# Kernel tuning notes

Hardware: AMD Instinct MI355X
Metric: run time of the kernel (lower is better)

Reference implementation:

```python
import jax, jax.numpy as jnp
import numpy as np

REL_DIM = 1024
NUM_HEADS = 16
HEAD_DIM = REL_DIM // NUM_HEADS
REL_EMB_DIM = 256
B, K = 32, 512
SCALE = 1.0 / float(np.sqrt(HEAD_DIM))


def setup_inputs() -> dict:
    key = jax.random.key(0)
    ks = jax.random.split(key, 7)
    s = 1.0 / float(np.sqrt(REL_DIM))
    return {
        "h_R": jax.random.normal(ks[0], (B, K, REL_DIM), dtype=jnp.float32),
        "R": jax.random.normal(ks[1], (K, REL_EMB_DIM), dtype=jnp.float32),
        "W_q": jax.random.normal(ks[2], (REL_DIM, REL_DIM), dtype=jnp.float32) * s,
        "W_k": jax.random.normal(ks[3], (REL_DIM, REL_DIM), dtype=jnp.float32) * s,
        "W_v": jax.random.normal(ks[4], (REL_DIM, REL_DIM), dtype=jnp.float32) * s,
        "W_o": jax.random.normal(ks[5], (REL_DIM, REL_DIM), dtype=jnp.float32) * s,
        "w_sim": jax.random.normal(ks[6], (NUM_HEADS,), dtype=jnp.float32) * 0.1,
    }


def reference(h_R, R, W_q, W_k, W_v, W_o, w_sim):
    Bb, Kk, _ = h_R.shape
    H, D = NUM_HEADS, HEAD_DIM
    # torch Linear: x @ W.T ; then split heads -> (B, H, K, D)
    def proj(x, W):
        return jnp.einsum('bkd,ed->bke', x, W).reshape(Bb, Kk, H, D).transpose(0, 2, 1, 3)
    q = proj(h_R, W_q)
    k = proj(h_R, W_k)
    v = proj(h_R, W_v)
    attn = jnp.einsum('bhqd,bhkd->bhqk', q, k) * SCALE
    # cosine-similarity bias (batch-independent): (H, K, K)
    R_norm = R / jnp.maximum(jnp.linalg.norm(R, axis=-1, keepdims=True), 1e-12)
    sim = R_norm @ R_norm.T  # (K, K)
    bias = w_sim[:, None, None] * sim[None]  # (H, K, K)
    attn = attn + bias[None]
    alpha = jax.nn.softmax(attn, axis=-1)
    out = jnp.einsum('bhqk,bhkd->bhqd', alpha, v)
    out = out.transpose(0, 2, 1, 3).reshape(Bb, Kk, H * D)
    return jnp.einsum('bkd,ed->bke', out, W_o)
```

## Files before the change

kernel.cpp:

```cpp
#include <hip/hip_runtime.h>

#define SEQK 512
#define NH 16
#define HD 64
#define RD 1024
#define BBATCH 32
#define QK_SCALE 0.125f

typedef unsigned short u16;
using bf16x8 = __attribute__((ext_vector_type(8))) short;
using f32x4  = __attribute__((ext_vector_type(4))) float;

__device__ __forceinline__ u16 f2bf(float f) {
  unsigned u = __float_as_uint(f);
  u += 0x7FFFu + ((u >> 16) & 1u);
  return (u16)(u >> 16);
}
__device__ __forceinline__ u16 f2bf_fast(float f) {
  return (u16)((__float_as_uint(f) + 0x8000u) >> 16);
}
__device__ __forceinline__ float bf2f(u16 v) {
  return __uint_as_float(((unsigned)v) << 16);
}

__device__ __forceinline__ void async_cp16(const void* g, void* l) {
  __builtin_amdgcn_global_load_lds(
      (__attribute__((address_space(1))) void*)(void*)g,
      (__attribute__((address_space(3))) void*)l,
      16, 0, 0);
}

__global__ void convert_kernel(const float* __restrict__ hR,
                               const float* __restrict__ Wq, const float* __restrict__ Wk,
                               const float* __restrict__ Wv, const float* __restrict__ Wo,
                               u16* __restrict__ hR16,
                               u16* __restrict__ Wq16, u16* __restrict__ Wk16,
                               u16* __restrict__ Wv16, u16* __restrict__ Wo16) {
  size_t i4 = (size_t)blockIdx.x * blockDim.x + threadIdx.x;
  size_t e = i4 * 4;
  const float* src; u16* dst; size_t off;
  if (e < 16777216u) { src = hR; dst = hR16; off = e; }
  else {
    size_t r = e - 16777216u;
    int w = (int)(r >> 20);
    off = r & 1048575u;
    src = (w == 0 ? Wq : w == 1 ? Wk : w == 2 ? Wv : Wo);
    dst = (w == 0 ? Wq16 : w == 1 ? Wk16 : w == 2 ? Wv16 : Wo16);
  }
  float4 v = *(const float4*)(src + off);
  ushort4 o;
  o.x = f2bf(v.x); o.y = f2bf(v.y); o.z = f2bf(v.z); o.w = f2bf(v.w);
  *(ushort4*)(dst + off) = o;
}

__global__ void rnorm_kernel(const float* __restrict__ R, float* __restrict__ Rn) {
  int row = blockIdx.x;
  int lane = threadIdx.x;
  float4 v = *(const float4*)(R + (size_t)row * 256 + lane * 4);
  float ss = v.x * v.x + v.y * v.y + v.z * v.z + v.w * v.w;
  for (int off = 32; off; off >>= 1) ss += __shfl_xor(ss, off);
  float s = 1.0f / fmaxf(sqrtf(ss), 1e-12f);
  float4 o = {v.x * s, v.y * s, v.z * s, v.w * s};
  *(float4*)(Rn + (size_t)row * 256 + lane * 4) = o;
}

__global__ void sim_kernel(const float* __restrict__ Rn, u16* __restrict__ sim16) {
  __shared__ float Rl[16 * 256];
  int i0 = blockIdx.x * 16;
  int t = threadIdx.x;
  #pragma unroll
  for (int i = 0; i < 4; i++) {
    int f = t + i * 256;
    *(float4*)&Rl[f * 4] = *(const float4*)(Rn + (size_t)i0 * 256 + f * 4);
  }
  __syncthreads();
  int j = blockIdx.y * 64 + (t & 63);
  int iq = t >> 6;
  float acc[4] = {0.f, 0.f, 0.f, 0.f};
  for (int c = 0; c < 64; c++) {
    float4 rv = *(const float4*)(Rn + (size_t)j * 256 + c * 4);
    #pragma unroll
    for (int i2 = 0; i2 < 4; i2++) {
      float4 a = *(const float4*)&Rl[(iq * 4 + i2) * 256 + c * 4];
      acc[i2] += a.x * rv.x + a.y * rv.y + a.z * rv.z + a.w * rv.w;
    }
  }
  #pragma unroll
  for (int i2 = 0; i2 < 4; i2++)
    sim16[(size_t)(i0 + iq * 4 + i2) * 512 + j] = f2bf(acc[i2]);
}

template <int MODE>
__global__ __launch_bounds__(256)
void gemm_kernel(const u16* __restrict__ A,
                 const u16* __restrict__ B0, const u16* __restrict__ B1,
                 const u16* __restrict__ B2,
                 u16* __restrict__ q16, u16* __restrict__ k16, u16* __restrict__ vt16,
                 float* __restrict__ outF) {
  __shared__ u16 Alds[128 * 32];
  __shared__ u16 Blds[128 * 32];
  int tid = threadIdx.x;
  int wave = tid >> 6, lane = tid & 63;
  int wm = wave & 1, wn = wave >> 1;
  int lr = lane & 15, qd = lane >> 4;
  int mb = blockIdx.x * 128;
  int ny = blockIdx.y;

  const u16* Bmat;
  int nbmat;
  if (MODE == 0) {
    int wsel = ny >> 3;
    Bmat = (wsel == 0 ? B0 : wsel == 1 ? B1 : B2);
    nbmat = (ny & 7) * 128;
  } else {
    Bmat = B0;
    nbmat = ny * 128;
  }

  f32x4 zero = {0.f, 0.f, 0.f, 0.f};
  f32x4 acc[4][4];
  #pragma unroll
  for (int i = 0; i < 4; i++)
    #pragma unroll
    for (int j = 0; j < 4; j++) acc[i][j] = zero;

  for (int kb = 0; kb < 1024; kb += 32) {
    #pragma unroll
    for (int j = 0; j < 2; j++) {
      int r = (wave * 2 + j) * 16 + (lane >> 2);
      int c = (lane & 3) ^ ((r >> 1) & 3);
      async_cp16(A + (size_t)(mb + r) * 1024 + kb + c * 8,
                 &Alds[(wave * 2 + j) * 512]);
      async_cp16(Bmat + (size_t)(nbmat + r) * 1024 + kb + c * 8,
                 &Blds[(wave * 2 + j) * 512]);
    }
    __syncthreads();

    bf16x8 af[4], bf[4];
    #pragma unroll
    for (int mi = 0; mi < 4; mi++) {
      int ra = wm * 64 + mi * 16 + lr;
      af[mi] = *(const bf16x8*)&Alds[ra * 32 + ((qd ^ ((ra >> 1) & 3)) << 3)];
      int rb = wn * 64 + mi * 16 + lr;
      bf[mi] = *(const bf16x8*)&Blds[rb * 32 + ((qd ^ ((rb >> 1) & 3)) << 3)];
    }
    #pragma unroll
    for (int mi = 0; mi < 4; mi++)
      #pragma unroll
      for (int ni = 0; ni < 4; ni++)
        acc[mi][ni] = __builtin_amdgcn_mfma_f32_16x16x32_bf16(af[mi], bf[ni],
                                                              acc[mi][ni], 0, 0, 0);
    __syncthreads();
  }

  if (MODE == 0) {
    int wsel = ny >> 3;
    if (wsel == 2) {
      #pragma unroll
      for (int mi = 0; mi < 4; mi++) {
        int m = mb + wm * 64 + mi * 16 + qd * 4;
        int b = m >> 9, kk = m & 511;
        #pragma unroll
        for (int ni = 0; ni < 4; ni++) {
          int n = nbmat + wn * 64 + ni * 16 + lr;
          int h = n >> 6, d = n & 63;
          ushort4 o4;
          o4.x = f2bf(acc[mi][ni][0]); o4.y = f2bf(acc[mi][ni][1]);
          o4.z = f2bf(acc[mi][ni][2]); o4.w = f2bf(acc[mi][ni][3]);
          *(ushort4*)(vt16 + ((size_t)(b * 16 + h) * 64 + d) * 512 + kk) = o4;
        }
      }
    } else {
      u16* dst = (wsel == 0 ? q16 : k16);
      float scl = (wsel == 0) ? QK_SCALE : 1.0f;
      #pragma unroll
      for (int mi = 0; mi < 4; mi++) {
        int m = mb + wm * 64 + mi * 16 + qd * 4;
        int b = m >> 9, kk = m & 511;
        #pragma unroll
        for (int ni = 0; ni < 4; ni++) {
          int n = nbmat + wn * 64 + ni * 16 + lr;
          int h = n >> 6, d = n & 63;
          u16* p = dst + ((size_t)(b * 16 + h) * 512 + kk) * 64 + d;
          #pragma unroll
          for (int r = 0; r < 4; r++) p[(size_t)r * 64] = f2bf(acc[mi][ni][r] * scl);
        }
      }
    }
  } else {
    #pragma unroll
    for (int mi = 0; mi < 4; mi++) {
      int m = mb + wm * 64 + mi * 16 + qd * 4;
      #pragma unroll
      for (int ni = 0; ni < 4; ni++) {
        int n = ny * 128 + wn * 64 + ni * 16 + lr;
        #pragma unroll
        for (int r = 0; r < 4; r++) outF[(size_t)(m + r) * 1024 + n] = acc[mi][ni][r];
      }
    }
  }
}

__global__ __launch_bounds__(256, 6)
void attn_kernel(const u16* __restrict__ q16, const u16* __restrict__ k16,
                 const u16* __restrict__ vt16, const u16* __restrict__ sim16,
                 const float* __restrict__ wsim, u16* __restrict__ attn16) {
  __shared__ u16 Kbuf[64 * 64];
  __shared__ u16 Vbuf[64 * 64];
  __shared__ u16 Plds[4 * 1152];

  int id = blockIdx.x;
  int xcd = id & 7;
  int j = id >> 3;
  int qt = j & 7;
  int bh = xcd * 64 + (j >> 3);
  int b = bh >> 4, h = bh & 15;

  int tid = threadIdx.x;
  int wave = tid >> 6, lane = tid & 63;
  int lr = lane & 15, qd = lane >> 4;
  int qrb = qt * 64 + wave * 16;
  u16* Pw = &Plds[wave * 1152];
  int pkey_r = (lr ^ (lr >> 1)) & 7;

  const u16* qp = q16 + ((size_t)bh * 512 + qrb + lr) * 64 + qd * 8;
  bf16x8 aq0 = *(const bf16x8*)qp;
  bf16x8 aq1 = *(const bf16x8*)(qp + 32);

  float ws = wsim[h];
  int row0 = qrb + qd * 4;

  f32x4 zero = {0.f, 0.f, 0.f, 0.f};
  f32x4 o[4];
  #pragma unroll
  for (int nt = 0; nt < 4; nt++) o[nt] = zero;
  float l_run[4] = {0.f, 0.f, 0.f, 0.f};

  const u16* kbase = k16 + (size_t)bh * 512 * 64;
  const u16* vbase = vt16 + (size_t)bh * 64 * 512;
  int lrow = lane >> 3, lchk = lane & 7;

  for (int ck = 0; ck < 8; ck++) {
    int k0 = ck * 64;
    __syncthreads();
    #pragma unroll
    for (int jj = 0; jj < 2; jj++) {
      int rb = wave * 16 + jj * 8;
      int r = rb + lrow;
      async_cp16(kbase + (size_t)(k0 + r) * 64 + ((lchk ^ (r & 7)) << 3),
                 &Kbuf[rb * 64]);
    }
    #pragma unroll
    for (int jj = 0; jj < 2; jj++) {
      int db = wave * 16 + jj * 8;
      int d = db + lrow;
      async_cp16(vbase + (size_t)d * 512 + k0 + ((lchk ^ (d & 7)) << 3),
                 &Vbuf[db * 64]);
    }
    __syncthreads();

    f32x4 s[4];
    #pragma unroll
    for (int jt = 0; jt < 4; jt++) {
      int kl = jt * 16 + lr;
      ushort4 b4 = *(const ushort4*)(sim16 + (size_t)(k0 + kl) * 512 + row0);
      f32x4 t = {ws * bf2f(b4.x), ws * bf2f(b4.y), ws * bf2f(b4.z), ws * bf2f(b4.w)};
      const u16* krow = &Kbuf[kl * 64];
      int sw = kl & 7;
      bf16x8 kf0 = *(const bf16x8*)(krow + ((qd ^ sw) << 3));
      bf16x8 kf1 = *(const bf16x8*)(krow + (((qd + 4) ^ sw) << 3));
      t = __builtin_amdgcn_mfma_f32_16x16x32_bf16(aq0, kf0, t, 0, 0, 0);
      t = __builtin_amdgcn_mfma_f32_16x16x32_bf16(aq1, kf1, t, 0, 0, 0);
      s[jt] = t;
    }
    #pragma unroll
    for (int jt = 0; jt < 4; jt++) {
      int c = jt * 2 + (lr >> 3);
      #pragma unroll
      for (int r = 0; r < 4; r++) {
        float e = __expf(s[jt][r]);
        l_run[r] += e;
        int row = qd * 4 + r;
        int key = (row ^ (row >> 1)) & 7;
        Pw[row * 64 + (((c ^ key) & 7) << 3) + (lr & 7)] = f2bf_fast(e);
      }
    }
    #pragma unroll
    for (int ks = 0; ks < 2; ks++) {
      bf16x8 ap = *(const bf16x8*)&Pw[lr * 64 + ((((ks * 4 + qd) ^ pkey_r) & 7) << 3)];
      #pragma unroll
      for (int nt = 0; nt < 4; nt++) {
        int d = nt * 16 + lr;
        bf16x8 vf = *(const bf16x8*)&Vbuf[d * 64 + ((((ks * 4 + qd) ^ (d & 7)) & 7) << 3)];
        o[nt] = __builtin_amdgcn_mfma_f32_16x16x32_bf16(ap, vf, o[nt], 0, 0, 0);
      }
    }
  }

  float inv[4];
  #pragma unroll
  for (int r = 0; r < 4; r++) {
    float t = l_run[r];
    t += __shfl_xor(t, 1); t += __shfl_xor(t, 2);
    t += __shfl_xor(t, 4); t += __shfl_xor(t, 8);
    inv[r] = 1.0f / t;
  }
  u16* Ow = Pw;
  #pragma unroll
  for (int nt = 0; nt < 4; nt++)
    #pragma unroll
    for (int r = 0; r < 4; r++)
      Ow[(qd * 4 + r) * 72 + nt * 16 + lr] = f2bf_fast(o[nt][r] * inv[r]);
  #pragma unroll
  for (int it = 0; it < 2; it++) {
    int row = it * 8 + (lane >> 3);
    int seg = lane & 7;
    bf16x8 val = *(const bf16x8*)&Ow[row * 72 + seg * 8];
    *(bf16x8*)(attn16 + ((size_t)b * 512 + qrb + row) * 1024 + h * 64 + seg * 8) = val;
  }
}

extern "C" void kernel_launch(void* const* d_in, const int* in_sizes, int n_in,
                              void* d_out, int out_size, void* d_ws, size_t ws_size,
                              hipStream_t stream) {
  const float* hR  = (const float*)d_in[0];
  const float* R   = (const float*)d_in[1];
  const float* Wq  = (const float*)d_in[2];
  const float* Wk  = (const float*)d_in[3];
  const float* Wv  = (const float*)d_in[4];
  const float* Wo  = (const float*)d_in[5];
  const float* wsm = (const float*)d_in[6];
  float* out = (float*)d_out;

  const size_t NE = 16777216;
  u16* ws16   = (u16*)d_ws;
  u16* hR16   = ws16;
  u16* attn16 = ws16;
  u16* q16    = ws16 + NE;
  u16* k16    = ws16 + 2 * NE;
  u16* vt16   = ws16 + 3 * NE;
  u16* Wq16   = ws16 + 4 * NE;
  u16* Wk16   = Wq16 + 1048576;
  u16* Wv16   = Wk16 + 1048576;
  u16* Wo16   = Wv16 + 1048576;
  u16* sim16  = Wo16 + 1048576;
  float* Rn   = (float*)(sim16 + 262144);

  convert_kernel<<<20480, 256, 0, stream>>>(hR, Wq, Wk, Wv, Wo,
                                            hR16, Wq16, Wk16, Wv16, Wo16);
  rnorm_kernel<<<512, 64, 0, stream>>>(R, Rn);
  sim_kernel<<<dim3(32, 8), 256, 0, stream>>>(Rn, sim16);
  gemm_kernel<0><<<dim3(128, 24), 256, 0, stream>>>(hR16, Wq16, Wk16, Wv16,
                                                    q16, k16, vt16, nullptr);
  attn_kernel<<<4096, 256, 0, stream>>>(q16, k16, vt16, sim16, wsm, attn16);
  gemm_kernel<1><<<dim3(128, 8), 256, 0, stream>>>(attn16, Wo16, nullptr, nullptr,
                                                   nullptr, nullptr, nullptr, out);
}
```

Measured before the change: 500.9 us.

## Process all queries of a batch-head per attention block to reuse K/V tiles

```diff
diff --git a/kernel.cpp b/kernel.cpp
--- a/kernel.cpp
+++ b/kernel.cpp
@@ -201,122 +201,130 @@
   }
 }
 
-__global__ __launch_bounds__(256, 6)
+__global__ __launch_bounds__(256, 2)
 void attn_kernel(const u16* __restrict__ q16, const u16* __restrict__ k16,
                  const u16* __restrict__ vt16, const u16* __restrict__ sim16,
                  const float* __restrict__ wsim, u16* __restrict__ attn16) {
-  __shared__ u16 Kbuf[64 * 64];
-  __shared__ u16 Vbuf[64 * 64];
-  __shared__ u16 Plds[4 * 1152];
+  __shared__ u16 Kbuf[128 * 64];
+  __shared__ u16 Vbuf[64 * 128];
+  __shared__ u16 Plds[4 * 2048];
 
   int id = blockIdx.x;
-  int xcd = id & 7;
-  int j = id >> 3;
-  int qt = j & 7;
-  int bh = xcd * 64 + (j >> 3);
+  int bh = (id & 7) * 64 + (id >> 3);
   int b = bh >> 4, h = bh & 15;
 
   int tid = threadIdx.x;
   int wave = tid >> 6, lane = tid & 63;
   int lr = lane & 15, qd = lane >> 4;
-  int qrb = qt * 64 + wave * 16;
-  u16* Pw = &Plds[wave * 1152];
-  int pkey_r = (lr ^ (lr >> 1)) & 7;
-
-  const u16* qp = q16 + ((size_t)bh * 512 + qrb + lr) * 64 + qd * 8;
-  bf16x8 aq0 = *(const bf16x8*)qp;
-  bf16x8 aq1 = *(const bf16x8*)(qp + 32);
+  u16* Pw = &Plds[wave * 2048];
 
   float ws = wsim[h];
-  int row0 = qrb + qd * 4;
-
-  f32x4 zero = {0.f, 0.f, 0.f, 0.f};
-  f32x4 o[4];
-  #pragma unroll
-  for (int nt = 0; nt < 4; nt++) o[nt] = zero;
-  float l_run[4] = {0.f, 0.f, 0.f, 0.f};
-
   const u16* kbase = k16 + (size_t)bh * 512 * 64;
   const u16* vbase = vt16 + (size_t)bh * 64 * 512;
-  int lrow = lane >> 3, lchk = lane & 7;
-
-  for (int ck = 0; ck < 8; ck++) {
-    int k0 = ck * 64;
+  const u16* qbase = q16 + (size_t)bh * 512 * 64;
+
+  f32x4 zero = {0.f, 0.f, 0.f, 0.f};
+  f32x4 o[8][4];
+  #pragma unroll
+  for (int t = 0; t < 8; t++)
+    #pragma unroll
+    for (int nt = 0; nt < 4; nt++) o[t][nt] = zero;
+  float l_run[8][4];
+  #pragma unroll
+  for (int t = 0; t < 8; t++)
+    #pragma unroll
+    for (int r = 0; r < 4; r++) l_run[t][r] = 0.f;
+
+  for (int ck = 0; ck < 4; ck++) {
+    int k0 = ck * 128;
     __syncthreads();
     #pragma unroll
-    for (int jj = 0; jj < 2; jj++) {
-      int rb = wave * 16 + jj * 8;
-      int r = rb + lrow;
-      async_cp16(kbase + (size_t)(k0 + r) * 64 + ((lchk ^ (r & 7)) << 3),
-                 &Kbuf[rb * 64]);
-    }
-    #pragma unroll
-    for (int jj = 0; jj < 2; jj++) {
-      int db = wave * 16 + jj * 8;
-      int d = db + lrow;
-      async_cp16(vbase + (size_t)d * 512 + k0 + ((lchk ^ (d & 7)) << 3),
-                 &Vbuf[db * 64]);
+    for (int jj = 0; jj < 4; jj++) {
+      int rb = wave * 32 + jj * 8;
+      int r = rb + (lane >> 3);
+      int c = (lane & 7) ^ (r & 7);
+      async_cp16(kbase + (size_t)(k0 + r) * 64 + c * 8, &Kbuf[rb * 64]);
+    }
+    #pragma unroll
+    for (int jj = 0; jj < 4; jj++) {
+      int db = wave * 16 + jj * 4;
+      int d = db + (lane >> 4);
+      int c = (lane & 15) ^ (d & 15);
+      async_cp16(vbase + (size_t)d * 512 + k0 + c * 8, &Vbuf[db * 128]);
     }
     __syncthreads();
 
-    f32x4 s[4];
-    #pragma unroll
-    for (int jt = 0; jt < 4; jt++) {
-      int kl = jt * 16 + lr;
-      ushort4 b4 = *(const ushort4*)(sim16 + (size_t)(k0 + kl) * 512 + row0);
-      f32x4 t = {ws * bf2f(b4.x), ws * bf2f(b4.y), ws * bf2f(b4.z), ws * bf2f(b4.w)};
-      const u16* krow = &Kbuf[kl * 64];
-      int sw = kl & 7;
-      bf16x8 kf0 = *(const bf16x8*)(krow + ((qd ^ sw) << 3));
-      bf16x8 kf1 = *(const bf16x8*)(krow + (((qd + 4) ^ sw) << 3));
-      t = __builtin_amdgcn_mfma_f32_16x16x32_bf16(aq0, kf0, t, 0, 0, 0);
-      t = __builtin_amdgcn_mfma_f32_16x16x32_bf16(aq1, kf1, t, 0, 0, 0);
-      s[jt] = t;
-    }
-    #pragma unroll
-    for (int jt = 0; jt < 4; jt++) {
-      int c = jt * 2 + (lr >> 3);
-      #pragma unroll
-      for (int r = 0; r < 4; r++) {
-        float e = __expf(s[jt][r]);
-        l_run[r] += e;
-        int row = qd * 4 + r;
-        int key = (row ^ (row >> 1)) & 7;
-        Pw[row * 64 + (((c ^ key) & 7) << 3) + (lr & 7)] = f2bf_fast(e);
-      }
-    }
-    #pragma unroll
-    for (int ks = 0; ks < 2; ks++) {
-      bf16x8 ap = *(const bf16x8*)&Pw[lr * 64 + ((((ks * 4 + qd) ^ pkey_r) & 7) << 3)];
-      #pragma unroll
-      for (int nt = 0; nt < 4; nt++) {
-        int d = nt * 16 + lr;
-        bf16x8 vf = *(const bf16x8*)&Vbuf[d * 64 + ((((ks * 4 + qd) ^ (d & 7)) & 7) << 3)];
-        o[nt] = __builtin_amdgcn_mfma_f32_16x16x32_bf16(ap, vf, o[nt], 0, 0, 0);
-      }
-    }
-  }
-
-  float inv[4];
-  #pragma unroll
-  for (int r = 0; r < 4; r++) {
-    float t = l_run[r];
-    t += __shfl_xor(t, 1); t += __shfl_xor(t, 2);
-    t += __shfl_xor(t, 4); t += __shfl_xor(t, 8);
-    inv[r] = 1.0f / t;
-  }
-  u16* Ow = Pw;
-  #pragma unroll
-  for (int nt = 0; nt < 4; nt++)
-    #pragma unroll
-    for (int r = 0; r < 4; r++)
-      Ow[(qd * 4 + r) * 72 + nt * 16 + lr] = f2bf_fast(o[nt][r] * inv[r]);
-  #pragma unroll
-  for (int it = 0; it < 2; it++) {
-    int row = it * 8 + (lane >> 3);
-    int seg = lane & 7;
-    bf16x8 val = *(const bf16x8*)&Ow[row * 72 + seg * 8];
-    *(bf16x8*)(attn16 + ((size_t)b * 512 + qrb + row) * 1024 + h * 64 + seg * 8) = val;
+    #pragma unroll
+    for (int t = 0; t < 8; t++) {
+      int qrb = wave * 128 + t * 16;
+      int row0 = qrb + qd * 4;
+      const u16* qp = qbase + (size_t)(qrb + lr) * 64 + qd * 8;
+      bf16x8 aq0 = *(const bf16x8*)qp;
+      bf16x8 aq1 = *(const bf16x8*)(qp + 32);
+
+      f32x4 s[8];
+      #pragma unroll
+      for (int jt = 0; jt < 8; jt++) {
+        int kl = jt * 16 + lr;
+        ushort4 b4 = *(const ushort4*)(sim16 + (size_t)(k0 + kl) * 512 + row0);
+        f32x4 tt = {ws * bf2f(b4.x), ws * bf2f(b4.y), ws * bf2f(b4.z), ws * bf2f(b4.w)};
+        const u16* krow = &Kbuf[kl * 64];
+        int sw = kl & 7;
+        bf16x8 kf0 = *(const bf16x8*)(krow + ((qd ^ sw) << 3));
+        bf16x8 kf1 = *(const bf16x8*)(krow + (((qd + 4) ^ sw) << 3));
+        tt = __builtin_amdgcn_mfma_f32_16x16x32_bf16(aq0, kf0, tt, 0, 0, 0);
+        tt = __builtin_amdgcn_mfma_f32_16x16x32_bf16(aq1, kf1, tt, 0, 0, 0);
+        s[jt] = tt;
+      }
+      #pragma unroll
+      for (int jt = 0; jt < 8; jt++) {
+        int c = jt * 2 + (lr >> 3);
+        int e = lr & 7;
+        #pragma unroll
+        for (int r = 0; r < 4; r++) {
+          float ev = __expf(s[jt][r]);
+          l_run[t][r] += ev;
+          int row = qd * 4 + r;
+          Pw[row * 128 + ((c ^ row) & 15) * 8 + e] = f2bf_fast(ev);
+        }
+      }
+      #pragma unroll
+      for (int ks = 0; ks < 4; ks++) {
+        bf16x8 ap = *(const bf16x8*)&Pw[lr * 128 + (((ks * 4 + qd) ^ lr) & 15) * 8];
+        #pragma unroll
+        for (int nt = 0; nt < 4; nt++) {
+          int d = nt * 16 + lr;
+          bf16x8 vf = *(const bf16x8*)&Vbuf[d * 128 + (((ks * 4 + qd) ^ (d & 15)) << 3)];
+          o[t][nt] = __builtin_amdgcn_mfma_f32_16x16x32_bf16(ap, vf, o[t][nt], 0, 0, 0);
+        }
+      }
+    }
+  }
+
+  #pragma unroll
+  for (int t = 0; t < 8; t++) {
+    int qrb = wave * 128 + t * 16;
+    float inv[4];
+    #pragma unroll
+    for (int r = 0; r < 4; r++) {
+      float tt = l_run[t][r];
+      tt += __shfl_xor(tt, 1); tt += __shfl_xor(tt, 2);
+      tt += __shfl_xor(tt, 4); tt += __shfl_xor(tt, 8);
+      inv[r] = 1.0f / tt;
+    }
+    u16* Ow = Pw;
+    #pragma unroll
+    for (int nt = 0; nt < 4; nt++)
+      #pragma unroll
+      for (int r = 0; r < 4; r++)
+        Ow[(qd * 4 + r) * 72 + nt * 16 + lr] = f2bf_fast(o[t][nt][r] * inv[r]);
+    #pragma unroll
+    for (int it = 0; it < 2; it++) {
+      int row = it * 8 + (lane >> 3);
+      int seg = lane & 7;
+      bf16x8 val = *(const bf16x8*)&Ow[row * 72 + seg * 8];
+      *(bf16x8*)(attn16 + ((size_t)b * 512 + qrb + row) * 1024 + h * 64 + seg * 8) = val;
+    }
   }
 }
 
@@ -352,7 +360,7 @@
   sim_kernel<<<dim3(32, 8), 256, 0, stream>>>(Rn, sim16);
   gemm_kernel<0><<<dim3(128, 24), 256, 0, stream>>>(hR16, Wq16, Wk16, Wv16,
                                                     q16, k16, vt16, nullptr);
-  attn_kernel<<<4096, 256, 0, stream>>>(q16, k16, vt16, sim16, wsm, attn16);
+  attn_kernel<<<512, 256, 0, stream>>>(q16, k16, vt16, sim16, wsm, attn16);
   gemm_kernel<1><<<dim3(128, 8), 256, 0, stream>>>(attn16, Wo16, nullptr, nullptr,
                                                    nullptr, nullptr, nullptr, out);
 }
```

After: 515.7 us. 1.03x slower.
